# Kernel tuning notes

Measured on AMD Instinct MI355X. Metric: run time of the kernel, lower is better.

The kernel has to match this reference:

```python
import jax, jax.numpy as jnp
import numpy as np

EPS = 1e-3  # keras BatchNormalization default epsilon


def _dwconv_t(y, w):
    # depthwise conv along time (axis 1), SAME padding. y:(B,T,S,G,n), w:(G,n,k)
    k = w.shape[-1]
    T = y.shape[1]
    pl = (k - 1) // 2
    yp = jnp.pad(y, ((0, 0), (pl, k - 1 - pl), (0, 0), (0, 0), (0, 0)))
    return sum(yp[:, j:j + T] * w[..., j] for j in range(k))


def _tc_layer(x, w, b, k3, k5, k7, gamma, beta, mu, var):
    # x:(B,T,S,C); w:(5,G,Cg,nb); b/gamma/beta/mu/var:(5,G,nb); k*:(G,nb,k)
    B, T, S, C = x.shape
    G, nb = w.shape[1], w.shape[-1]
    # global spatial pooling: concat [x, max, mean] along spatial axis -> S+2
    x = jnp.concatenate([x, x.max(axis=2, keepdims=True), x.mean(axis=2, keepdims=True)], axis=2)
    S = S + 2
    xg = x.reshape(B, T, S, G, C // G)
    # 5 grouped 1x1x1 pointwise convs at once
    y = jnp.einsum('btsgc,pgcn->pbtsgn', xg, w) + b[:, None, None, None]
    t0 = y[0]
    t3 = _dwconv_t(y[1], k3)
    t5 = _dwconv_t(y[2], k5)
    t7 = _dwconv_t(y[3], k7)
    # temporal maxpool pool=2 stride=1 SAME (TF pads right)
    t1 = jnp.maximum(y[4], jnp.concatenate([y[4][:, 1:], y[4][:, -1:]], axis=1))
    ts = jnp.stack([t0, t3, t5, t7, t1])  # (5,B,T,S,G,nb)
    scale = gamma[:, None, None, None] / jnp.sqrt(var[:, None, None, None] + EPS)
    ts = (ts - mu[:, None, None, None]) * scale + beta[:, None, None, None]
    # concat branches within each group: (B,T,S,G,5*nb)
    z = jnp.transpose(ts, (1, 2, 3, 4, 0, 5)).reshape(B, T, S, G, 5 * nb)
    z = jax.nn.relu(z)
    # channel shuffle: (G, per) -> (per, G) -> flatten
    z = jnp.swapaxes(z, -1, -2).reshape(B, T, S, G * 5 * nb)
    # MaxPooling3D pool=(2,1,1) stride 2 valid: halve T
    return jnp.maximum(z[:, 0::2], z[:, 1::2])


def setup_inputs() -> dict:
    key = jax.random.key(0)
    ks = jax.random.split(key, 32)
    B, T, H, W, C = 16, 64, 7, 7, 1024
    G = 8
    d = {'x': jax.random.normal(ks[0], (B, T, H, W, C), jnp.float32)}
    specs = [(0, 128, 32), (1, 160, 40)]  # (layer, Cg, nb)
    i = 1
    for l, cg, nb in specs:
        d[f'w{l}'] = 0.02 * jax.random.normal(ks[i], (5, G, cg, nb)); i += 1
        d[f'b{l}'] = 0.02 * jax.random.normal(ks[i], (5, G, nb)); i += 1
        d[f'k3_{l}'] = 0.1 * jax.random.normal(ks[i], (G, nb, 3)); i += 1
        d[f'k5_{l}'] = 0.1 * jax.random.normal(ks[i], (G, nb, 5)); i += 1
        d[f'k7_{l}'] = 0.1 * jax.random.normal(ks[i], (G, nb, 7)); i += 1
        d[f'g{l}'] = jax.random.uniform(ks[i], (5, G, nb), minval=0.5, maxval=1.5); i += 1
        d[f'be{l}'] = 0.02 * jax.random.normal(ks[i], (5, G, nb)); i += 1
        d[f'mu{l}'] = 0.02 * jax.random.normal(ks[i], (5, G, nb)); i += 1
        d[f'v{l}'] = jax.random.uniform(ks[i], (5, G, nb), minval=0.5, maxval=1.5); i += 1
    return d


def reference(x, w0, b0, k3_0, k5_0, k7_0, g0, be0, mu0, v0,
              w1, b1, k3_1, k5_1, k7_1, g1, be1, mu1, v1):
    B, T, H, W, C = x.shape
    z = x.reshape(B, T, H * W, C)  # (B,T,S,C), side_dim2=1 kept implicit
    z = _tc_layer(z, w0, b0, k3_0, k5_0, k7_0, g0, be0, mu0, v0)
    z = _tc_layer(z, w1, b1, k3_1, k5_1, k7_1, g1, be1, mu1, v1)
    return z[:, :, :, None, :]  # (B, T/4, S+4, 1, Cout)
```

## Files before the change

### kernel.cpp

```cpp
#include <hip/hip_runtime.h>
#include <hip/hip_bf16.h>

#define EPSBN 1e-3f

typedef __attribute__((ext_vector_type(8))) short bf16x8;
typedef __attribute__((ext_vector_type(8))) unsigned short ushort8;
typedef __attribute__((ext_vector_type(4))) float f32x4;


__device__ __forceinline__ float bf2f(unsigned short u) {
    union { unsigned int i; float f; } c; c.i = (unsigned int)u << 16; return c.f;
}
__device__ __forceinline__ unsigned short f2bf(float f) {
    union { float f; unsigned int i; } c; c.f = f;
    unsigned int r = c.i + 0x7FFF + ((c.i >> 16) & 1);
    return (unsigned short)(r >> 16);
}

__global__ __launch_bounds__(256) void tc_prep_reduce0(
    const float* __restrict__ x, unsigned short* __restrict__ extb,
    const float* __restrict__ w0, const float* __restrict__ w1,
    unsigned short* __restrict__ W0t, unsigned short* __restrict__ W1t)
{
    if (blockIdx.x < 1024) {
        const int bt = blockIdx.x;
        const int b  = bt >> 6, t = bt & 63;
        const int c  = threadIdx.x * 4;
        const float4* src = reinterpret_cast<const float4*>(x + (size_t)bt * 49 * 1024 + c);
        float4 v = src[0];
        float mx0 = v.x, mx1 = v.y, mx2 = v.z, mx3 = v.w;
        float sm0 = v.x, sm1 = v.y, sm2 = v.z, sm3 = v.w;
        for (int s = 1; s < 49; ++s) {
            float4 u = src[(size_t)s * 256];
            mx0 = fmaxf(mx0, u.x); sm0 += u.x;
            mx1 = fmaxf(mx1, u.y); sm1 += u.y;
            mx2 = fmaxf(mx2, u.z); sm2 += u.z;
            mx3 = fmaxf(mx3, u.w); sm3 += u.w;
        }
        const float inv = 1.0f / 49.0f;
        ushort4 omx, omn;
        omx.x=f2bf(mx0); omx.y=f2bf(mx1); omx.z=f2bf(mx2); omx.w=f2bf(mx3);
        omn.x=f2bf(sm0*inv); omn.y=f2bf(sm1*inv); omn.z=f2bf(sm2*inv); omn.w=f2bf(sm3*inv);
        *reinterpret_cast<ushort4*>(&extb[((size_t)(b*2 + 0)*64 + t)*1024 + c]) = omx;
        *reinterpret_cast<ushort4*>(&extb[((size_t)(b*2 + 1)*64 + t)*1024 + c]) = omn;
    } else {
        const int idx = (blockIdx.x - 1024) * 256 + threadIdx.x;
        if (idx < 163840) {
            const int g   = idx / 20480;
            const int rem = idx - g*20480;
            const int n   = rem >> 7;
            const int k   = rem & 127;
            const int p   = n >> 5, nn = n & 31;
            W0t[idx] = f2bf(w0[(((size_t)p*8 + g)*128 + k)*32 + nn]);
        } else if (idx < 163840 + 256000) {
            const int i2  = idx - 163840;
            const int g   = i2 / 32000;
            const int rem = i2 - g*32000;
            const int n   = rem / 160;
            const int k   = rem - n*160;
            const int kref = (k % 20)*8 + k/20;
            const int p   = n / 40, nn = n - p*40;
            W1t[i2] = f2bf(w1[(((size_t)p*8 + g)*160 + kref)*40 + nn]);
        }
    }
}

__global__ __launch_bounds__(512, 6) void tc_layer0(
    const float* __restrict__ x, const unsigned short* __restrict__ extb,
    const unsigned short* __restrict__ W0t, const float* __restrict__ bias,
    const float* __restrict__ k3, const float* __restrict__ k5,
    const float* __restrict__ k7,
    const float* __restrict__ gam, const float* __restrict__ bet,
    const float* __restrict__ mu, const float* __restrict__ var,
    unsigned short* __restrict__ zb)
{
    const int tid = threadIdx.x;
    const int g   = blockIdx.x / 416;
    const int rem = blockIdx.x % 416;
    const int sp  = rem % 26;
    const int b   = rem / 26;
    const int s0  = sp*2;
    const int has1 = (s0 + 1 < 51);

    __shared__ __align__(16) unsigned short lds[128*136 + 160*40];
    unsigned short* AtU = lds;
    unsigned short* WtU = lds + 128*136;
    unsigned short* Ytb = lds;

    #pragma unroll
    for (int it = 0; it < 4; ++it) {
        const int fid = tid + it*512;
        const int row = fid >> 4;
        const int ch8 = (fid & 15) * 8;
        const int t   = row & 63;
        const int s   = (row < 64) ? s0 : (has1 ? s0+1 : s0);
        ushort8 u;
        if (s < 49) {
            const float* sp_ = x + ((size_t)(b*64 + t)*49 + s)*1024 + g*128 + ch8;
            const float4 f0 = *reinterpret_cast<const float4*>(sp_);
            const float4 f1 = *reinterpret_cast<const float4*>(sp_ + 4);
            u[0]=f2bf(f0.x); u[1]=f2bf(f0.y); u[2]=f2bf(f0.z); u[3]=f2bf(f0.w);
            u[4]=f2bf(f1.x); u[5]=f2bf(f1.y); u[6]=f2bf(f1.z); u[7]=f2bf(f1.w);
        } else {
            u = *reinterpret_cast<const ushort8*>(
                &extb[((size_t)(b*2 + (s-49))*64 + t)*1024 + g*128 + ch8]);
        }
        *reinterpret_cast<ushort8*>(&AtU[row*136 + ch8]) = u;
    }

    const int lane = tid & 63;
    const int wid  = tid >> 6;
    const int fr   = lane & 15;
    const int kb   = lane >> 4;

    f32x4 zero = {0.f, 0.f, 0.f, 0.f};
    f32x4 acc[10];
    #pragma unroll
    for (int i = 0; i < 10; ++i) acc[i] = zero;

    for (int kc = 0; kc < 4; ++kc) {
        __syncthreads();
        #pragma unroll
        for (int it = 0; it < 2; ++it) {
            const int gi = tid + it*512;
            if (gi < 640) {
                const int n = gi >> 2, part = (gi & 3) * 8;
                *reinterpret_cast<ushort8*>(&WtU[n*40 + part]) =
                    *reinterpret_cast<const ushort8*>(
                        &W0t[((size_t)g*160 + n)*128 + kc*32 + part]);
            }
        }
        __syncthreads();
        const bf16x8 bfrag = *reinterpret_cast<const bf16x8*>(
            &AtU[(wid*16 + fr)*136 + kc*32 + kb*8]);
        #pragma unroll
        for (int nt = 0; nt < 10; ++nt) {
            const bf16x8 afrag = *reinterpret_cast<const bf16x8*>(
                &WtU[(nt*16 + fr)*40 + kb*8]);
            acc[nt] = __builtin_amdgcn_mfma_f32_16x16x32_bf16(afrag, bfrag, acc[nt], 0, 0, 0);
        }
    }
    __syncthreads();
    #pragma unroll
    for (int nt = 0; nt < 10; ++nt)
        #pragma unroll
        for (int r = 0; r < 4; ++r)
            Ytb[(nt*16 + kb*4 + r)*134 + wid*16 + fr] = f2bf(acc[nt][r]);
    __syncthreads();

    #pragma unroll
    for (int it2 = 0; it2 < 2; ++it2) {
        const int task = tid + it2*512;
        if (task < 640) {
            const int ch   = task % 160;
            const int rest = task / 160;
            const int sIdx = rest >> 1;
            const int th   = rest & 1;
            if (!sIdx || has1) {
                const int s  = s0 + sIdx;
                const int p  = ch >> 5, n = ch & 31;
                const int pi = (p*8 + g)*32 + n;
                const float bsv = bias[pi];
                const float sc  = gam[pi]*rsqrtf(var[pi]+EPSBN);
                const float sh  = bet[pi] - mu[pi]*sc;
                const int t0 = th*32 - 4;
                float yw[40];
                #pragma unroll
                for (int i = 0; i < 40; i += 2) {
                    const int t = t0 + i;
                    if (t >= 0 && t < 64) {
                        const unsigned int w2 = *reinterpret_cast<const unsigned int*>(
                            &Ytb[ch*134 + sIdx*64 + t]);
                        yw[i]   = bf2f((unsigned short)(w2 & 0xffffu)) + bsv;
                        yw[i+1] = bf2f((unsigned short)(w2 >> 16)) + bsv;
                    } else { yw[i] = 0.f; yw[i+1] = 0.f; }
                }
                unsigned short* zp = zb + ((size_t)(b*32)*53 + s)*1280 + g*160 + ch
                                   + (size_t)(th*16)*67840;
                if (p == 0) {
                    #pragma unroll
                    for (int q2 = 0; q2 < 16; ++q2) {
                        const float r = fmaxf(fmaxf(fmaf(yw[2*q2+4],sc,sh),
                                                    fmaf(yw[2*q2+5],sc,sh)), 0.f);
                        zp[(size_t)q2*67840] = f2bf(r);
                    }
                } else if (p == 1) {
                    float wk[3];
                    #pragma unroll
                    for (int j = 0; j < 3; ++j) wk[j] = k3[(g*32+n)*3+j];
                    #pragma unroll
                    for (int q2 = 0; q2 < 16; ++q2) {
                        float vv[2];
                        #pragma unroll
                        for (int q = 0; q < 2; ++q) {
                            float v = 0.f;
                            #pragma unroll
                            for (int j = 0; j < 3; ++j)
                                v = fmaf(yw[2*q2 + q + j + 3], wk[j], v);
                            vv[q] = v;
                        }
                        const float r = fmaxf(fmaxf(fmaf(vv[0],sc,sh), fmaf(vv[1],sc,sh)), 0.f);
                        zp[(size_t)q2*67840] = f2bf(r);
                    }
                } else if (p == 2) {
                    float wk[5];
                    #pragma unroll
                    for (int j = 0; j < 5; ++j) wk[j] = k5[(g*32+n)*5+j];
                    #pragma unroll
                    for (int q2 = 0; q2 < 16; ++q2) {
                        float vv[2];
                        #pragma unroll
                        for (int q = 0; q < 2; ++q) {
                            float v = 0.f;
                            #pragma unroll
                            for (int j = 0; j < 5; ++j)
                                v = fmaf(yw[2*q2 + q + j + 2], wk[j], v);
                            vv[q] = v;
                        }
                        const float r = fmaxf(fmaxf(fmaf(vv[0],sc,sh), fmaf(vv[1],sc,sh)), 0.f);
                        zp[(size_t)q2*67840] = f2bf(r);
                    }
                } else if (p == 3) {
                    float wk[7];
                    #pragma unroll
                    for (int j = 0; j < 7; ++j) wk[j] = k7[(g*32+n)*7+j];
                    #pragma unroll
                    for (int q2 = 0; q2 < 16; ++q2) {
                        float vv[2];
                        #pragma unroll
                        for (int q = 0; q < 2; ++q) {
                            float v = 0.f;
                            #pragma unroll
                            for (int j = 0; j < 7; ++j)
                                v = fmaf(yw[2*q2 + q + j + 1], wk[j], v);
                            vv[q] = v;
                        }
                        const float r = fmaxf(fmaxf(fmaf(vv[0],sc,sh), fmaf(vv[1],sc,sh)), 0.f);
                        zp[(size_t)q2*67840] = f2bf(r);
                    }
                } else {
                    #pragma unroll
                    for (int q2 = 0; q2 < 16; ++q2) {
                        const int tq = th*16 + q2;
                        const float v0 = fmaxf(yw[2*q2+4], yw[2*q2+5]);
                        const float vb = (2*tq+2 < 64) ? yw[2*q2+6] : yw[35];
                        const float v1 = fmaxf(yw[2*q2+5], vb);
                        const float r = fmaxf(fmaxf(fmaf(v0,sc,sh), fmaf(v1,sc,sh)), 0.f);
                        zp[(size_t)q2*67840] = f2bf(r);
                    }
                }
            }
        }
    }
}

__global__ __launch_bounds__(320) void tc_reduce1(unsigned short* __restrict__ zb) {
    const int bt = blockIdx.x;
    const int c  = threadIdx.x * 4;
    unsigned short* base = zb + (size_t)bt * 67840;
    ushort4 u = *reinterpret_cast<const ushort4*>(&base[c]);
    float v0 = bf2f(u.x), v1 = bf2f(u.y), v2 = bf2f(u.z), v3 = bf2f(u.w);
    float mx0 = v0, mx1 = v1, mx2 = v2, mx3 = v3;
    float sm0 = v0, sm1 = v1, sm2 = v2, sm3 = v3;
    for (int s = 1; s < 51; ++s) {
        ushort4 w = *reinterpret_cast<const ushort4*>(&base[(size_t)s*1280 + c]);
        v0 = bf2f(w.x); v1 = bf2f(w.y); v2 = bf2f(w.z); v3 = bf2f(w.w);
        mx0 = fmaxf(mx0, v0); sm0 += v0;
        mx1 = fmaxf(mx1, v1); sm1 += v1;
        mx2 = fmaxf(mx2, v2); sm2 += v2;
        mx3 = fmaxf(mx3, v3); sm3 += v3;
    }
    const float inv = 1.0f / 51.0f;
    ushort4 o;
    o.x = f2bf(mx0); o.y = f2bf(mx1); o.z = f2bf(mx2); o.w = f2bf(mx3);
    *reinterpret_cast<ushort4*>(&base[(size_t)51*1280 + c]) = o;
    o.x = f2bf(sm0*inv); o.y = f2bf(sm1*inv); o.z = f2bf(sm2*inv); o.w = f2bf(sm3*inv);
    *reinterpret_cast<ushort4*>(&base[(size_t)52*1280 + c]) = o;
}

__global__ __launch_bounds__(512, 4) void tc_layer1(
    const unsigned short* __restrict__ zbi,
    const unsigned short* __restrict__ W1t, const float* __restrict__ bias,
    const float* __restrict__ k3, const float* __restrict__ k5,
    const float* __restrict__ k7,
    const float* __restrict__ gam, const float* __restrict__ bet,
    const float* __restrict__ mu, const float* __restrict__ var,
    unsigned short* __restrict__ og)
{
    const int tid = threadIdx.x;
    const int g   = blockIdx.x / 224;
    const int rem = blockIdx.x % 224;
    const int sq  = rem % 14;
    const int b   = rem / 14;
    const int s0  = sq*4;
    const int ns  = (53 - s0 < 4) ? (53 - s0) : 4;

    __shared__ __align__(16) unsigned short lds[26000];
    unsigned short* AhU = lds;
    unsigned short* WtU = lds + 13312;
    unsigned short* Ytb = lds;

    if (tid < 40) {
        ushort8 z8 = {0,0,0,0,0,0,0,0};
        const int r = tid / 5, cp = tid - r*5;
        *reinterpret_cast<ushort8*>(&WtU[(200 + r)*40 + cp*8]) = z8;
    }

    #pragma unroll
    for (int it = 0; it < 6; ++it) {
        const int fid = tid + it*512;
        const int row = fid / 24;
        const int seg = fid - row*24;
        const int gg  = seg / 5, q = seg - gg*5;
        const int ch  = gg*160 + g*20 + q*4;
        const int sl  = row >> 5;
        const int s   = s0 + ((sl < ns) ? sl : 0);
        const int t   = row & 31;
        const unsigned short* src = zbi + ((size_t)(b*32 + t)*53 + s)*1280 + ch;
        *reinterpret_cast<ushort4*>(&AhU[row*104 + seg*4]) =
            *reinterpret_cast<const ushort4*>(src);
    }

    const int lane = tid & 63;
    const int wid  = tid >> 6;
    const int fr   = lane & 15;
    const int kb   = lane >> 4;

    f32x4 zero = {0.f, 0.f, 0.f, 0.f};
    f32x4 acc[13];
    #pragma unroll
    for (int i = 0; i < 13; ++i) acc[i] = zero;

    for (int kc = 0; kc < 5; ++kc) {
        __syncthreads();
        if (kc == 3) {
            #pragma unroll
            for (int it = 0; it < 4; ++it) {
                const int fid = tid + it*512;
                const int row = fid >> 4;
                const int s24 = fid & 15;
                const int seg = s24 + 24;
                const int gg  = seg / 5, q = seg - gg*5;
                const int ch  = gg*160 + g*20 + q*4;
                const int sl  = row >> 5;
                const int s   = s0 + ((sl < ns) ? sl : 0);
                const int t   = row & 31;
                const unsigned short* src = zbi + ((size_t)(b*32 + t)*53 + s)*1280 + ch;
                *reinterpret_cast<ushort4*>(&AhU[row*72 + s24*4]) =
                    *reinterpret_cast<const ushort4*>(src);
            }
        }
        #pragma unroll
        for (int it = 0; it < 2; ++it) {
            const int gi = tid + it*512;
            if (gi < 800) {
                const int n = gi >> 2, part = (gi & 3) * 8;
                *reinterpret_cast<ushort8*>(&WtU[n*40 + part]) =
                    *reinterpret_cast<const ushort8*>(
                        &W1t[((size_t)g*200 + n)*160 + kc*32 + part]);
            }
        }
        __syncthreads();
        const bf16x8 bfrag = (kc < 3)
            ? *reinterpret_cast<const bf16x8*>(&AhU[(wid*16 + fr)*104 + kc*32 + kb*8])
            : *reinterpret_cast<const bf16x8*>(&AhU[(wid*16 + fr)*72 + (kc-3)*32 + kb*8]);
        #pragma unroll
        for (int nt = 0; nt < 13; ++nt) {
            const bf16x8 afrag = *reinterpret_cast<const bf16x8*>(
                &WtU[(nt*16 + fr)*40 + kb*8]);
            acc[nt] = __builtin_amdgcn_mfma_f32_16x16x32_bf16(afrag, bfrag, acc[nt], 0, 0, 0);
        }
    }
    __syncthreads();
    #pragma unroll
    for (int nt = 0; nt < 13; ++nt) {
        #pragma unroll
        for (int r = 0; r < 4; ++r) {
            const int n = nt*16 + kb*4 + r;
            if (n < 200) Ytb[n*130 + wid*16 + fr] = f2bf(acc[nt][r]);
        }
    }
    __syncthreads();

    #pragma unroll
    for (int it = 0; it < 2; ++it) {
        const int task = tid + it*512;
        if (task < 800) {
            const int sIdx = task / 200;
            const int ch   = task - sIdx*200;
            if (sIdx < ns) {
                const int s  = s0 + sIdx;
                const int p  = ch / 40, n = ch - p*40;
                const int pi = (p*8 + g)*40 + n;
                const float bsv = bias[pi];
                const float sc  = gam[pi]*rsqrtf(var[pi]+EPSBN);
                const float sh  = bet[pi] - mu[pi]*sc;
                float yv[32];
                #pragma unroll
                for (int i = 0; i < 16; ++i) {
                    const unsigned int w2 = *reinterpret_cast<const unsigned int*>(
                        &Ytb[ch*130 + sIdx*32 + i*2]);
                    yv[2*i]   = bf2f((unsigned short)(w2 & 0xffffu)) + bsv;
                    yv[2*i+1] = bf2f((unsigned short)(w2 >> 16)) + bsv;
                }
                unsigned short* op = og + ((size_t)(b*16)*53 + s)*1600 + g*200 + ch;
                if (p == 0) {
                    #pragma unroll
                    for (int tq = 0; tq < 16; ++tq) {
                        const float r = fmaxf(fmaxf(fmaf(yv[2*tq],sc,sh), fmaf(yv[2*tq+1],sc,sh)), 0.f);
                        op[(size_t)tq*84800] = f2bf(r);
                    }
                } else if (p == 1) {
                    const float w0_ = k3[(g*40+n)*3+0], w1_ = k3[(g*40+n)*3+1], w2_ = k3[(g*40+n)*3+2];
                    #pragma unroll
                    for (int tq = 0; tq < 16; ++tq) {
                        float a = yv[2*tq]*w1_;
                        if (tq > 0) a = fmaf(yv[2*tq-1], w0_, a);
                        a = fmaf(yv[2*tq+1], w2_, a);
                        float c2 = fmaf(yv[2*tq], w0_, yv[2*tq+1]*w1_);
                        if (tq < 15) c2 = fmaf(yv[2*tq+2], w2_, c2);
                        const float r = fmaxf(fmaxf(fmaf(a,sc,sh), fmaf(c2,sc,sh)), 0.f);
                        op[(size_t)tq*84800] = f2bf(r);
                    }
                } else if (p == 2) {
                    float wk[5];
                    #pragma unroll
                    for (int j = 0; j < 5; ++j) wk[j] = k5[(g*40+n)*5+j];
                    #pragma unroll
                    for (int tq = 0; tq < 16; ++tq) {
                        float vv[2];
                        #pragma unroll
                        for (int q = 0; q < 2; ++q) {
                            const int t = 2*tq + q;
                            float v = 0.f;
                            #pragma unroll
                            for (int j = 0; j < 5; ++j) {
                                const int ttp = t + j - 2;
                                if (ttp >= 0 && ttp < 32) v = fmaf(yv[ttp], wk[j], v);
                            }
                            vv[q] = v;
                        }
                        const float r = fmaxf(fmaxf(fmaf(vv[0],sc,sh), fmaf(vv[1],sc,sh)), 0.f);
                        op[(size_t)tq*84800] = f2bf(r);
                    }
                } else if (p == 3) {
                    float wk[7];
                    #pragma unroll
                    for (int j = 0; j < 7; ++j) wk[j] = k7[(g*40+n)*7+j];
                    #pragma unroll
                    for (int tq = 0; tq < 16; ++tq) {
                        float vv[2];
                        #pragma unroll
                        for (int q = 0; q < 2; ++q) {
                            const int t = 2*tq + q;
                            float v = 0.f;
                            #pragma unroll
                            for (int j = 0; j < 7; ++j) {
                                const int ttp = t + j - 3;
                                if (ttp >= 0 && ttp < 32) v = fmaf(yv[ttp], wk[j], v);
                            }
                            vv[q] = v;
                        }
                        const float r = fmaxf(fmaxf(fmaf(vv[0],sc,sh), fmaf(vv[1],sc,sh)), 0.f);
                        op[(size_t)tq*84800] = f2bf(r);
                    }
                } else {
                    #pragma unroll
                    for (int tq = 0; tq < 16; ++tq) {
                        const float v0 = fmaxf(yv[2*tq], yv[2*tq+1]);
                        const float v1 = fmaxf(yv[2*tq+1], yv[(2*tq+2 < 32) ? 2*tq+2 : 31]);
                        const float r = fmaxf(fmaxf(fmaf(v0,sc,sh), fmaf(v1,sc,sh)), 0.f);
                        op[(size_t)tq*84800] = f2bf(r);
                    }
                }
            }
        }
    }
}

__global__ __launch_bounds__(256) void tc_shuffle(const unsigned short* __restrict__ og,
                                                  float* __restrict__ o) {
    __shared__ unsigned short row[1600];
    const size_t base = (size_t)blockIdx.x * 1600;
    const int tid = threadIdx.x;
    if (tid < 200)
        *reinterpret_cast<ushort8*>(&row[tid*8]) =
            *reinterpret_cast<const ushort8*>(&og[base + (size_t)tid*8]);
    __syncthreads();
    #pragma unroll
    for (int it = 0; it < 2; ++it) {
        const int f4 = tid + it*256;
        if (f4 < 400) {
            const int c = f4*4;
            float4 v;
            v.x = bf2f(row[((c  ) & 7)*200 + ((c  ) >> 3)]);
            v.y = bf2f(row[((c+1) & 7)*200 + ((c+1) >> 3)]);
            v.z = bf2f(row[((c+2) & 7)*200 + ((c+2) >> 3)]);
            v.w = bf2f(row[((c+3) & 7)*200 + ((c+3) >> 3)]);
            *reinterpret_cast<float4*>(&o[base + (size_t)c]) = v;
        }
    }
}

extern "C" void kernel_launch(void* const* d_in, const int* in_sizes, int n_in,
                              void* d_out, int out_size, void* d_ws, size_t ws_size,
                              hipStream_t stream) {
    const float* x    = (const float*)d_in[0];
    const float* w0   = (const float*)d_in[1];
    const float* b0   = (const float*)d_in[2];
    const float* k3_0 = (const float*)d_in[3];
    const float* k5_0 = (const float*)d_in[4];
    const float* k7_0 = (const float*)d_in[5];
    const float* g0   = (const float*)d_in[6];
    const float* be0  = (const float*)d_in[7];
    const float* mu0  = (const float*)d_in[8];
    const float* v0   = (const float*)d_in[9];
    const float* w1   = (const float*)d_in[10];
    const float* b1   = (const float*)d_in[11];
    const float* k3_1 = (const float*)d_in[12];
    const float* k5_1 = (const float*)d_in[13];
    const float* k7_1 = (const float*)d_in[14];
    const float* g1   = (const float*)d_in[15];
    const float* be1  = (const float*)d_in[16];
    const float* mu1  = (const float*)d_in[17];
    const float* v1   = (const float*)d_in[18];

    const size_t n_zb   = 34734080;
    const size_t n_W0t  = 163840;
    const size_t n_W1t  = 256000;
    const size_t n_extb = 2097152;

    unsigned short* zb   = (unsigned short*)d_ws;
    unsigned short* W0t  = zb + n_zb;
    unsigned short* W1t  = W0t + n_W0t;
    unsigned short* extb = W1t + n_W1t;
    unsigned short* og   = extb + n_extb;

    tc_prep_reduce0<<<1024 + 1640, 256, 0, stream>>>(x, extb, w0, w1, W0t, W1t);
    tc_layer0 <<<416*8, 512, 0, stream>>>(x, extb, W0t, b0, k3_0, k5_0,
                                          k7_0, g0, be0, mu0, v0, zb);
    tc_reduce1<<<16*32, 320, 0, stream>>>(zb);
    tc_layer1 <<<224*8, 512, 0, stream>>>(zb, W1t, b1, k3_1, k5_1, k7_1,
                                          g1, be1, mu1, v1, og);
    tc_shuffle<<<16*16*53, 256, 0, stream>>>(og, (float*)d_out);
}
```

Measured before the change: 237.3 us.

## Split layer-1 blocks to two spatial positions and split N tiles across wave pairs

The layer-1 kernel now processes 2 spatial positions per block instead of 4, doubling the grid. Each pair of waves shares one 16-row time tile and splits the 13 output N-tiles 7/6, so each wave holds 7 accumulators instead of 13. The whole 160-channel A slab is loaded once into LDS, removing the mid-loop reload at kc==3, and launch bounds are raised to allow 6 blocks per CU. The aim is higher occupancy and parallelism, at the cost of loading the weight matrix into LDS twice as many times in total and leaving some waves idle in the epilogue.

```diff
diff --git a/kernel.cpp b/kernel.cpp
--- a/kernel.cpp
+++ b/kernel.cpp
@@ -278,7 +278,7 @@
     *reinterpret_cast<ushort4*>(&base[(size_t)52*1280 + c]) = o;
 }
 
-__global__ __launch_bounds__(512, 4) void tc_layer1(
+__global__ __launch_bounds__(512, 6) void tc_layer1(
     const unsigned short* __restrict__ zbi,
     const unsigned short* __restrict__ W1t, const float* __restrict__ bias,
     const float* __restrict__ k3, const float* __restrict__ k5,
@@ -288,16 +288,16 @@
     unsigned short* __restrict__ og)
 {
     const int tid = threadIdx.x;
-    const int g   = blockIdx.x / 224;
-    const int rem = blockIdx.x % 224;
-    const int sq  = rem % 14;
-    const int b   = rem / 14;
-    const int s0  = sq*4;
-    const int ns  = (53 - s0 < 4) ? (53 - s0) : 4;
-
-    __shared__ __align__(16) unsigned short lds[26000];
-    unsigned short* AhU = lds;
-    unsigned short* WtU = lds + 13312;
+    const int g   = blockIdx.x / 432;
+    const int rem = blockIdx.x % 432;
+    const int sp  = rem % 27;
+    const int b   = rem / 27;
+    const int s0  = sp*2;
+    const int has1 = (s0 + 1 < 53);
+
+    __shared__ __align__(16) unsigned short lds[64*168 + 208*40];
+    unsigned short* AtU = lds;
+    unsigned short* WtU = lds + 64*168;
     unsigned short* Ytb = lds;
 
     if (tid < 40) {
@@ -307,49 +307,33 @@
     }
 
     #pragma unroll
-    for (int it = 0; it < 6; ++it) {
+    for (int it = 0; it < 5; ++it) {
         const int fid = tid + it*512;
-        const int row = fid / 24;
-        const int seg = fid - row*24;
+        const int row = fid / 40;
+        const int seg = fid - row*40;
         const int gg  = seg / 5, q = seg - gg*5;
         const int ch  = gg*160 + g*20 + q*4;
-        const int sl  = row >> 5;
-        const int s   = s0 + ((sl < ns) ? sl : 0);
+        const int s   = (row < 32) ? s0 : (has1 ? s0+1 : s0);
         const int t   = row & 31;
         const unsigned short* src = zbi + ((size_t)(b*32 + t)*53 + s)*1280 + ch;
-        *reinterpret_cast<ushort4*>(&AhU[row*104 + seg*4]) =
+        *reinterpret_cast<ushort4*>(&AtU[row*168 + seg*4]) =
             *reinterpret_cast<const ushort4*>(src);
     }
 
     const int lane = tid & 63;
     const int wid  = tid >> 6;
+    const int tt   = wid >> 1;
+    const int nh   = wid & 1;
     const int fr   = lane & 15;
     const int kb   = lane >> 4;
 
     f32x4 zero = {0.f, 0.f, 0.f, 0.f};
-    f32x4 acc[13];
-    #pragma unroll
-    for (int i = 0; i < 13; ++i) acc[i] = zero;
+    f32x4 acc[7];
+    #pragma unroll
+    for (int i = 0; i < 7; ++i) acc[i] = zero;
 
     for (int kc = 0; kc < 5; ++kc) {
         __syncthreads();
-        if (kc == 3) {
-            #pragma unroll
-            for (int it = 0; it < 4; ++it) {
-                const int fid = tid + it*512;
-                const int row = fid >> 4;
-                const int s24 = fid & 15;
-                const int seg = s24 + 24;
-                const int gg  = seg / 5, q = seg - gg*5;
-                const int ch  = gg*160 + g*20 + q*4;
-                const int sl  = row >> 5;
-                const int s   = s0 + ((sl < ns) ? sl : 0);
-                const int t   = row & 31;
-                const unsigned short* src = zbi + ((size_t)(b*32 + t)*53 + s)*1280 + ch;
-                *reinterpret_cast<ushort4*>(&AhU[row*72 + s24*4]) =
-                    *reinterpret_cast<const ushort4*>(src);
-            }
-        }
         #pragma unroll
         for (int it = 0; it < 2; ++it) {
             const int gi = tid + it*512;
@@ -361,117 +345,118 @@
             }
         }
         __syncthreads();
-        const bf16x8 bfrag = (kc < 3)
-            ? *reinterpret_cast<const bf16x8*>(&AhU[(wid*16 + fr)*104 + kc*32 + kb*8])
-            : *reinterpret_cast<const bf16x8*>(&AhU[(wid*16 + fr)*72 + (kc-3)*32 + kb*8]);
+        const bf16x8 bfrag = *reinterpret_cast<const bf16x8*>(
+            &AtU[(tt*16 + fr)*168 + kc*32 + kb*8]);
         #pragma unroll
-        for (int nt = 0; nt < 13; ++nt) {
-            const bf16x8 afrag = *reinterpret_cast<const bf16x8*>(
-                &WtU[(nt*16 + fr)*40 + kb*8]);
-            acc[nt] = __builtin_amdgcn_mfma_f32_16x16x32_bf16(afrag, bfrag, acc[nt], 0, 0, 0);
+        for (int i = 0; i < 7; ++i) {
+            const int nt = nh*7 + i;
+            if (nt < 13) {
+                const bf16x8 afrag = *reinterpret_cast<const bf16x8*>(
+                    &WtU[(nt*16 + fr)*40 + kb*8]);
+                acc[i] = __builtin_amdgcn_mfma_f32_16x16x32_bf16(afrag, bfrag, acc[i], 0, 0, 0);
+            }
         }
     }
     __syncthreads();
     #pragma unroll
-    for (int nt = 0; nt < 13; ++nt) {
-        #pragma unroll
-        for (int r = 0; r < 4; ++r) {
-            const int n = nt*16 + kb*4 + r;
-            if (n < 200) Ytb[n*130 + wid*16 + fr] = f2bf(acc[nt][r]);
+    for (int i = 0; i < 7; ++i) {
+        const int nt = nh*7 + i;
+        if (nt < 13) {
+            #pragma unroll
+            for (int r = 0; r < 4; ++r) {
+                const int n = nt*16 + kb*4 + r;
+                if (n < 200) Ytb[n*66 + tt*16 + fr] = f2bf(acc[i][r]);
+            }
         }
     }
     __syncthreads();
 
-    #pragma unroll
-    for (int it = 0; it < 2; ++it) {
-        const int task = tid + it*512;
-        if (task < 800) {
-            const int sIdx = task / 200;
-            const int ch   = task - sIdx*200;
-            if (sIdx < ns) {
-                const int s  = s0 + sIdx;
-                const int p  = ch / 40, n = ch - p*40;
-                const int pi = (p*8 + g)*40 + n;
-                const float bsv = bias[pi];
-                const float sc  = gam[pi]*rsqrtf(var[pi]+EPSBN);
-                const float sh  = bet[pi] - mu[pi]*sc;
-                float yv[32];
-                #pragma unroll
-                for (int i = 0; i < 16; ++i) {
-                    const unsigned int w2 = *reinterpret_cast<const unsigned int*>(
-                        &Ytb[ch*130 + sIdx*32 + i*2]);
-                    yv[2*i]   = bf2f((unsigned short)(w2 & 0xffffu)) + bsv;
-                    yv[2*i+1] = bf2f((unsigned short)(w2 >> 16)) + bsv;
-                }
-                unsigned short* op = og + ((size_t)(b*16)*53 + s)*1600 + g*200 + ch;
-                if (p == 0) {
-                    #pragma unroll
-                    for (int tq = 0; tq < 16; ++tq) {
-                        const float r = fmaxf(fmaxf(fmaf(yv[2*tq],sc,sh), fmaf(yv[2*tq+1],sc,sh)), 0.f);
-                        op[(size_t)tq*84800] = f2bf(r);
-                    }
-                } else if (p == 1) {
-                    const float w0_ = k3[(g*40+n)*3+0], w1_ = k3[(g*40+n)*3+1], w2_ = k3[(g*40+n)*3+2];
-                    #pragma unroll
-                    for (int tq = 0; tq < 16; ++tq) {
-                        float a = yv[2*tq]*w1_;
-                        if (tq > 0) a = fmaf(yv[2*tq-1], w0_, a);
-                        a = fmaf(yv[2*tq+1], w2_, a);
-                        float c2 = fmaf(yv[2*tq], w0_, yv[2*tq+1]*w1_);
-                        if (tq < 15) c2 = fmaf(yv[2*tq+2], w2_, c2);
-                        const float r = fmaxf(fmaxf(fmaf(a,sc,sh), fmaf(c2,sc,sh)), 0.f);
-                        op[(size_t)tq*84800] = f2bf(r);
-                    }
-                } else if (p == 2) {
-                    float wk[5];
-                    #pragma unroll
-                    for (int j = 0; j < 5; ++j) wk[j] = k5[(g*40+n)*5+j];
-                    #pragma unroll
-                    for (int tq = 0; tq < 16; ++tq) {
-                        float vv[2];
+    if (tid < 400) {
+        const int sIdx = tid / 200;
+        const int ch   = tid - sIdx*200;
+        if (!sIdx || has1) {
+            const int s  = s0 + sIdx;
+            const int p  = ch / 40, n = ch - p*40;
+            const int pi = (p*8 + g)*40 + n;
+            const float bsv = bias[pi];
+            const float sc  = gam[pi]*rsqrtf(var[pi]+EPSBN);
+            const float sh  = bet[pi] - mu[pi]*sc;
+            float yv[32];
+            #pragma unroll
+            for (int i = 0; i < 16; ++i) {
+                const unsigned int w2 = *reinterpret_cast<const unsigned int*>(
+                    &Ytb[ch*66 + sIdx*32 + i*2]);
+                yv[2*i]   = bf2f((unsigned short)(w2 & 0xffffu)) + bsv;
+                yv[2*i+1] = bf2f((unsigned short)(w2 >> 16)) + bsv;
+            }
+            unsigned short* op = og + ((size_t)(b*16)*53 + s)*1600 + g*200 + ch;
+            if (p == 0) {
+                #pragma unroll
+                for (int tq = 0; tq < 16; ++tq) {
+                    const float r = fmaxf(fmaxf(fmaf(yv[2*tq],sc,sh), fmaf(yv[2*tq+1],sc,sh)), 0.f);
+                    op[(size_t)tq*84800] = f2bf(r);
+                }
+            } else if (p == 1) {
+                const float w0_ = k3[(g*40+n)*3+0], w1_ = k3[(g*40+n)*3+1], w2_ = k3[(g*40+n)*3+2];
+                #pragma unroll
+                for (int tq = 0; tq < 16; ++tq) {
+                    float a = yv[2*tq]*w1_;
+                    if (tq > 0) a = fmaf(yv[2*tq-1], w0_, a);
+                    a = fmaf(yv[2*tq+1], w2_, a);
+                    float c2 = fmaf(yv[2*tq], w0_, yv[2*tq+1]*w1_);
+                    if (tq < 15) c2 = fmaf(yv[2*tq+2], w2_, c2);
+                    const float r = fmaxf(fmaxf(fmaf(a,sc,sh), fmaf(c2,sc,sh)), 0.f);
+                    op[(size_t)tq*84800] = f2bf(r);
+                }
+            } else if (p == 2) {
+                float wk[5];
+                #pragma unroll
+                for (int j = 0; j < 5; ++j) wk[j] = k5[(g*40+n)*5+j];
+                #pragma unroll
+                for (int tq = 0; tq < 16; ++tq) {
+                    float vv[2];
+                    #pragma unroll
+                    for (int q = 0; q < 2; ++q) {
+                        const int t = 2*tq + q;
+                        float v = 0.f;
                         #pragma unroll
-                        for (int q = 0; q < 2; ++q) {
-                            const int t = 2*tq + q;
-                            float v = 0.f;
-                            #pragma unroll
-                            for (int j = 0; j < 5; ++j) {
-                                const int ttp = t + j - 2;
-                                if (ttp >= 0 && ttp < 32) v = fmaf(yv[ttp], wk[j], v);
-                            }
-                            vv[q] = v;
+                        for (int j = 0; j < 5; ++j) {
+                            const int ttp = t + j - 2;
+                            if (ttp >= 0 && ttp < 32) v = fmaf(yv[ttp], wk[j], v);
                         }
-                        const float r = fmaxf(fmaxf(fmaf(vv[0],sc,sh), fmaf(vv[1],sc,sh)), 0.f);
-                        op[(size_t)tq*84800] = f2bf(r);
-                    }
-                } else if (p == 3) {
-                    float wk[7];
-                    #pragma unroll
-                    for (int j = 0; j < 7; ++j) wk[j] = k7[(g*40+n)*7+j];
-                    #pragma unroll
-                    for (int tq = 0; tq < 16; ++tq) {
-                        float vv[2];
+                        vv[q] = v;
+                    }
+                    const float r = fmaxf(fmaxf(fmaf(vv[0],sc,sh), fmaf(vv[1],sc,sh)), 0.f);
+                    op[(size_t)tq*84800] = f2bf(r);
+                }
+            } else if (p == 3) {
+                float wk[7];
+                #pragma unroll
+                for (int j = 0; j < 7; ++j) wk[j] = k7[(g*40+n)*7+j];
+                #pragma unroll
+                for (int tq = 0; tq < 16; ++tq) {
+                    float vv[2];
+                    #pragma unroll
+                    for (int q = 0; q < 2; ++q) {
+                        const int t = 2*tq + q;
+                        float v = 0.f;
                         #pragma unroll
-                        for (int q = 0; q < 2; ++q) {
-                            const int t = 2*tq + q;
-                            float v = 0.f;
-                            #pragma unroll
-                            for (int j = 0; j < 7; ++j) {
-                                const int ttp = t + j - 3;
-                                if (ttp >= 0 && ttp < 32) v = fmaf(yv[ttp], wk[j], v);
-                            }
-                            vv[q] = v;
+                        for (int j = 0; j < 7; ++j) {
+                            const int ttp = t + j - 3;
+                            if (ttp >= 0 && ttp < 32) v = fmaf(yv[ttp], wk[j], v);
                         }
-                        const float r = fmaxf(fmaxf(fmaf(vv[0],sc,sh), fmaf(vv[1],sc,sh)), 0.f);
-                        op[(size_t)tq*84800] = f2bf(r);
-                    }
-                } else {
-                    #pragma unroll
-                    for (int tq = 0; tq < 16; ++tq) {
-                        const float v0 = fmaxf(yv[2*tq], yv[2*tq+1]);
-                        const float v1 = fmaxf(yv[2*tq+1], yv[(2*tq+2 < 32) ? 2*tq+2 : 31]);
-                        const float r = fmaxf(fmaxf(fmaf(v0,sc,sh), fmaf(v1,sc,sh)), 0.f);
-                        op[(size_t)tq*84800] = f2bf(r);
-                    }
+                        vv[q] = v;
+                    }
+                    const float r = fmaxf(fmaxf(fmaf(vv[0],sc,sh), fmaf(vv[1],sc,sh)), 0.f);
+                    op[(size_t)tq*84800] = f2bf(r);
+                }
+            } else {
+                #pragma unroll
+                for (int tq = 0; tq < 16; ++tq) {
+                    const float v0 = fmaxf(yv[2*tq], yv[2*tq+1]);
+                    const float v1 = fmaxf(yv[2*tq+1], yv[(2*tq+2 < 32) ? 2*tq+2 : 31]);
+                    const float r = fmaxf(fmaxf(fmaf(v0,sc,sh), fmaf(v1,sc,sh)), 0.f);
+                    op[(size_t)tq*84800] = f2bf(r);
                 }
             }
         }
@@ -540,7 +525,7 @@
     tc_layer0 <<<416*8, 512, 0, stream>>>(x, extb, W0t, b0, k3_0, k5_0,
                                           k7_0, g0, be0, mu0, v0, zb);
     tc_reduce1<<<16*32, 320, 0, stream>>>(zb);
-    tc_layer1 <<<224*8, 512, 0, stream>>>(zb, W1t, b1, k3_1, k5_1, k7_1,
+    tc_layer1 <<<432*8, 512, 0, stream>>>(zb, W1t, b1, k3_1, k5_1, k7_1,
                                           g1, be1, mu1, v1, og);
     tc_shuffle<<<16*16*53, 256, 0, stream>>>(og, (float*)d_out);
 }
```

Result: slower. 242.4 us (+2.2%).
